# Kernel tuning notes

Measured on AMD Instinct MI355X. Metric: run time of the kernel, lower is better.

The kernel has to match this reference:

```python
import jax, jax.numpy as jnp
import numpy as np

N_NODES = 100000
N_EDGES = 800000
F_IN, HID, N_CLS = 256, 128, 32


def setup_inputs() -> dict:
    key = jax.random.key(0)
    k1, k2, k3, k4, k5 = jax.random.split(key, 5)
    features = jax.random.normal(k1, (N_NODES, F_IN), dtype=jnp.float32)
    # random directed edges with no self loops (so add_remaining_self_loops == append all loops)
    src = jax.random.randint(k2, (N_EDGES,), 0, N_NODES)
    off = jax.random.randint(k3, (N_EDGES,), 1, N_NODES)
    dst = (src + off) % N_NODES
    edge_index = jnp.stack([src, dst]).astype(jnp.int64)
    # Glorot-style params for the two GCNConv layers
    W1 = jax.random.normal(k4, (F_IN, HID), dtype=jnp.float32) * (1.0 / np.sqrt(F_IN))
    b1 = jnp.zeros((HID,), dtype=jnp.float32)
    W2 = jax.random.normal(k5, (HID, N_CLS), dtype=jnp.float32) * (1.0 / np.sqrt(HID))
    b2 = jnp.zeros((N_CLS,), dtype=jnp.float32)
    return {"features": features, "edge_index": edge_index, "W1": W1, "b1": b1, "W2": W2, "b2": b2}


def _gcn_conv(x, W, b, src, dst, norm, n):
    xw = x @ W                                  # [N, d_out] dense GEMM
    msg = xw[src] * norm[:, None]               # gather + scale, [E, d_out]
    out = jax.ops.segment_sum(msg, dst, num_segments=n)  # scatter-add to targets
    return out + b


def reference(features, edge_index, W1, b1, W2, b2):
    n = features.shape[0]
    # add_remaining_self_loops (input has none, so append all)
    loops = jnp.arange(n, dtype=edge_index.dtype)
    src = jnp.concatenate([edge_index[0], loops])
    dst = jnp.concatenate([edge_index[1], loops])
    # gcn_norm: deg over targets, sym normalization deg^-1/2 A deg^-1/2
    deg = jax.ops.segment_sum(jnp.ones_like(src, dtype=features.dtype), dst, num_segments=n)
    dinv = jnp.where(deg > 0, jax.lax.rsqrt(deg), 0.0)
    norm = dinv[src] * dinv[dst]
    x = _gcn_conv(features, W1, b1, src, dst, norm, n)
    x = jax.nn.relu(x)
    # dropout is identity at inference (training=False)
    x = _gcn_conv(x, W2, b2, src, dst, norm, n)
    return jax.nn.log_softmax(x, axis=1)
```

## Files before the change

### kernel.cpp

```cpp
#include <hip/hip_runtime.h>
#include <hip/hip_bf16.h>

typedef __bf16 bf16_t;
typedef __attribute__((ext_vector_type(8))) __bf16 bf16x8;
typedef __attribute__((ext_vector_type(4))) float f32x4;

__device__ inline void packB_one(const float* __restrict__ B, bf16_t* __restrict__ Bp,
                                 int N, int idx) {
    int j    = idx & 7;
    int lane = (idx >> 3) & 63;
    int st   = idx >> 9;
    int nt   = N >> 4;
    int s = st / nt, t = st - s * nt;
    int k = s * 32 + (lane >> 4) * 8 + j;
    int n = t * 16 + (lane & 15);
    Bp[idx] = (bf16_t)B[(size_t)k * N + n];
}

__global__ __launch_bounds__(256) void k_front(
        const float* __restrict__ feat, bf16_t* __restrict__ Ap,
        const float* __restrict__ W1, bf16_t* __restrict__ Bp1,
        const float* __restrict__ W2, bf16_t* __restrict__ Bp2,
        const int* __restrict__ dst, int* __restrict__ deg,
        int N_nodes, int E, int APACK_BLOCKS) {
    int b = blockIdx.x, t = threadIdx.x;
    if (b < APACK_BLOCKS) {
        int idx = b * 256 + t;
        if (idx >= N_nodes * 64) return;
        int w    = idx >> 6;
        int lane = idx & 63;
        int r16 = lane & 15, quad = lane >> 4;
        const float* arow = feat + (size_t)(w * 16 + r16) * 256 + quad * 8;
        bf16_t* opb = Ap + (size_t)w * 4096 + lane * 8;
#pragma unroll
        for (int s = 0; s < 8; ++s) {
            const float* ap = arow + s * 32;
            bf16x8 a;
#pragma unroll
            for (int j = 0; j < 8; ++j) a[j] = (bf16_t)ap[j];
            *(bf16x8*)(opb + s * 512) = a;
        }
        return;
    }
    b -= APACK_BLOCKS;
    const int PACK_BLOCKS = (32768 + 4096) / 256;
    if (b < PACK_BLOCKS) {
        int idx = b * 256 + t;
        if (idx < 32768) packB_one(W1, Bp1, 128, idx);
        else             packB_one(W2, Bp2, 32, idx - 32768);
        return;
    }
    int i = (b - PACK_BLOCKS) * 1024 + t * 4;
    if (i + 4 <= E) {
        int4 v = *(const int4*)(dst + i);
        atomicAdd(&deg[v.x], 1); atomicAdd(&deg[v.y], 1);
        atomicAdd(&deg[v.z], 1); atomicAdd(&deg[v.w], 1);
    } else {
#pragma unroll
        for (int j = 0; j < 4; ++j)
            if (i + j < E) atomicAdd(&deg[dst[i + j]], 1);
    }
}

__global__ __launch_bounds__(256) void k_dinv_scan1(const int* __restrict__ deg,
                                                    float* __restrict__ dinv,
                                                    int* __restrict__ bsum, int n) {
    __shared__ int red[256];
    int b = blockIdx.x, t = threadIdx.x;
    int base = b * 1024 + t * 4;
    int s = 0;
#pragma unroll
    for (int j = 0; j < 4; ++j) {
        int i = base + j;
        if (i < n) { int d = deg[i]; s += d; dinv[i] = rsqrtf((float)(d + 1)); }
    }
    red[t] = s;
    __syncthreads();
    for (int d = 128; d > 0; d >>= 1) {
        if (t < d) red[t] += red[t + d];
        __syncthreads();
    }
    if (t == 0) bsum[b] = red[0];
}

__global__ __launch_bounds__(256) void k_scan2(int* __restrict__ bsum, int nb,
                                               int* __restrict__ rowPtr, int n) {
    __shared__ int s[256];
    int t = threadIdx.x;
    int v = (t < nb) ? bsum[t] : 0;
    s[t] = v;
    __syncthreads();
    for (int d = 1; d < 256; d <<= 1) {
        int u = (t >= d) ? s[t - d] : 0;
        __syncthreads();
        s[t] += u;
        __syncthreads();
    }
    if (t < nb) bsum[t] = s[t] - v;
    if (t == 255) rowPtr[n] = s[255];
}

__global__ __launch_bounds__(256) void k_scan3(const int* __restrict__ deg,
                                               const int* __restrict__ bsum,
                                               int* __restrict__ rowPtr,
                                               int* __restrict__ cursor, int n) {
    __shared__ int red[256];
    int b = blockIdx.x, t = threadIdx.x;
    int base = b * 1024 + t * 4;
    int v[4]; int s = 0;
#pragma unroll
    for (int j = 0; j < 4; ++j) { int i = base + j; v[j] = (i < n) ? deg[i] : 0; s += v[j]; }
    red[t] = s;
    __syncthreads();
    for (int d = 1; d < 256; d <<= 1) {
        int u = (t >= d) ? red[t - d] : 0;
        __syncthreads();
        red[t] += u;
        __syncthreads();
    }
    int run = bsum[b] + red[t] - s;
#pragma unroll
    for (int j = 0; j < 4; ++j) {
        int i = base + j;
        if (i < n) { rowPtr[i] = run; cursor[i] = run; run += v[j]; }
    }
}

template <int KSTEPS, int NTILES>
__global__ __launch_bounds__(256) void k_gemm_scatter(
        const bf16_t* __restrict__ Ap, const bf16_t* __restrict__ Bp,
        bf16_t* __restrict__ C, int M, int gemmBlocks,
        const int* __restrict__ src, const int* __restrict__ dst,
        const float* __restrict__ dinv, int* __restrict__ cursor,
        int2* __restrict__ edata, int E) {
    int b = blockIdx.x, t = threadIdx.x;
    if (b < gemmBlocks) {
        int wave = (b * 256 + t) >> 6;
        if (wave * 16 >= M) return;
        int lane = t & 63;
        int r16 = lane & 15, quad = lane >> 4;
        const int N = NTILES * 16;
        f32x4 acc[NTILES] = {};
        const bf16_t* apb = Ap + (size_t)wave * (KSTEPS * 512) + lane * 8;
#pragma unroll
        for (int s = 0; s < KSTEPS; ++s) {
            bf16x8 a = *(const bf16x8*)(apb + s * 512);
            const bf16_t* bp = Bp + ((size_t)(s * NTILES) * 64 + lane) * 8;
#pragma unroll
            for (int tt = 0; tt < NTILES; ++tt) {
                bf16x8 bb = *(const bf16x8*)(bp + tt * 512);
                acc[tt] = __builtin_amdgcn_mfma_f32_16x16x32_bf16(a, bb, acc[tt], 0, 0, 0);
            }
        }
#pragma unroll
        for (int tt = 0; tt < NTILES; ++tt)
#pragma unroll
            for (int r = 0; r < 4; ++r)
                C[(size_t)(wave * 16 + quad * 4 + r) * N + tt * 16 + r16] = (bf16_t)acc[tt][r];
        return;
    }
    int e = (b - gemmBlocks) * 256 + t;
    if (e >= E) return;
    int s = src[e], d = dst[e];
    int pos = atomicAdd(&cursor[d], 1);
    int2 p; p.x = s; p.y = __float_as_int(dinv[s] * dinv[d]);
    edata[pos] = p;
}

template <int KSTEPS, int NTILES>
__global__ __launch_bounds__(256) void k_gemm_p(
        const bf16_t* __restrict__ Ap, const bf16_t* __restrict__ Bp,
        bf16_t* __restrict__ C, int M) {
    int wave = (blockIdx.x * blockDim.x + threadIdx.x) >> 6;
    if (wave * 16 >= M) return;
    int lane = threadIdx.x & 63;
    int r16 = lane & 15, quad = lane >> 4;
    const int N = NTILES * 16;
    f32x4 acc[NTILES] = {};
    const bf16_t* apb = Ap + (size_t)wave * (KSTEPS * 512) + lane * 8;
#pragma unroll
    for (int s = 0; s < KSTEPS; ++s) {
        bf16x8 a = *(const bf16x8*)(apb + s * 512);
        const bf16_t* bp = Bp + ((size_t)(s * NTILES) * 64 + lane) * 8;
#pragma unroll
        for (int t = 0; t < NTILES; ++t) {
            bf16x8 b = *(const bf16x8*)(bp + t * 512);
            acc[t] = __builtin_amdgcn_mfma_f32_16x16x32_bf16(a, b, acc[t], 0, 0, 0);
        }
    }
#pragma unroll
    for (int t = 0; t < NTILES; ++t)
#pragma unroll
        for (int r = 0; r < 4; ++r)
            C[(size_t)(wave * 16 + quad * 4 + r) * N + t * 16 + r16] = (bf16_t)acc[t][r];
}

__global__ __launch_bounds__(256) void k_agg1(
        const int* __restrict__ rowPtr, const int2* __restrict__ edata,
        const bf16_t* __restrict__ XW1, const float* __restrict__ dinv,
        const float* __restrict__ b1, bf16_t* __restrict__ Hp, int n) {
    int wave = (blockIdx.x * blockDim.x + threadIdx.x) >> 6;
    if (wave >= n) return;
    int lane = threadIdx.x & 63;
    int fl = (lane & 15) << 3;
    int h  = lane >> 4;
    int r0 = rowPtr[wave], r1 = rowPtr[wave + 1];
    float a0[8] = {}, a1[8] = {};
    int k = r0 + h;
    for (; k + 4 < r1; k += 8) {
        int2 e0 = edata[k], e1 = edata[k + 4];
        float w0 = __int_as_float(e0.y), w1 = __int_as_float(e1.y);
        bf16x8 x0 = *(const bf16x8*)(XW1 + ((size_t)e0.x << 7) + fl);
        bf16x8 x1 = *(const bf16x8*)(XW1 + ((size_t)e1.x << 7) + fl);
#pragma unroll
        for (int j = 0; j < 8; ++j) { a0[j] += (float)x0[j] * w0; a1[j] += (float)x1[j] * w1; }
    }
    if (k < r1) {
        int2 e0 = edata[k];
        float w0 = __int_as_float(e0.y);
        bf16x8 x0 = *(const bf16x8*)(XW1 + ((size_t)e0.x << 7) + fl);
#pragma unroll
        for (int j = 0; j < 8; ++j) a0[j] += (float)x0[j] * w0;
    }
#pragma unroll
    for (int j = 0; j < 8; ++j) {
        a0[j] += a1[j];
        a0[j] += __shfl_xor(a0[j], 16);
        a0[j] += __shfl_xor(a0[j], 32);
    }
    if (h == 0) {
        float d = dinv[wave], d2 = d * d;
        bf16x8 xs = *(const bf16x8*)(XW1 + ((size_t)wave << 7) + fl);
        bf16x8 hv;
#pragma unroll
        for (int j = 0; j < 8; ++j) {
            float v = a0[j] + (float)xs[j] * d2 + b1[fl + j];
            hv[j] = (bf16_t)fmaxf(v, 0.f);
        }
        int q = lane & 15;
        size_t off = (((size_t)(wave >> 4) * 4 + (q >> 2)) * 64
                      + (wave & 15) + 16 * (q & 3)) * 8;
        *(bf16x8*)(Hp + off) = hv;
    }
}

__global__ __launch_bounds__(256) void k_agg2(
        const int* __restrict__ rowPtr, const int2* __restrict__ edata,
        const bf16_t* __restrict__ XW2, const float* __restrict__ dinv,
        const float* __restrict__ b2, float* __restrict__ out, int n) {
    int wave = (blockIdx.x * blockDim.x + threadIdx.x) >> 6;
    if (wave >= n) return;
    int lane = threadIdx.x & 63;
    int g = lane & 15;
    int h = lane >> 4;
    int r0 = rowPtr[wave], r1 = rowPtr[wave + 1];
    float a00 = 0.f, a01 = 0.f, a10 = 0.f, a11 = 0.f;
    int k = r0 + h;
    for (; k + 4 < r1; k += 8) {
        int2 e0 = edata[k], e1 = edata[k + 4];
        float w0 = __int_as_float(e0.y), w1 = __int_as_float(e1.y);
        unsigned p0 = *(const unsigned*)(XW2 + ((size_t)e0.x << 5) + 2 * g);
        unsigned p1 = *(const unsigned*)(XW2 + ((size_t)e1.x << 5) + 2 * g);
        a00 += __int_as_float(p0 << 16) * w0;
        a01 += __int_as_float(p0 & 0xffff0000u) * w0;
        a10 += __int_as_float(p1 << 16) * w1;
        a11 += __int_as_float(p1 & 0xffff0000u) * w1;
    }
    if (k < r1) {
        int2 e0 = edata[k];
        float w0 = __int_as_float(e0.y);
        unsigned p0 = *(const unsigned*)(XW2 + ((size_t)e0.x << 5) + 2 * g);
        a00 += __int_as_float(p0 << 16) * w0;
        a01 += __int_as_float(p0 & 0xffff0000u) * w0;
    }
    float v0 = a00 + a10, v1 = a01 + a11;
    v0 += __shfl_xor(v0, 16); v0 += __shfl_xor(v0, 32);
    v1 += __shfl_xor(v1, 16); v1 += __shfl_xor(v1, 32);
    float d = dinv[wave], d2 = d * d;
    unsigned ps = *(const unsigned*)(XW2 + ((size_t)wave << 5) + 2 * g);
    float2 bb = *(const float2*)(b2 + 2 * g);
    v0 += __int_as_float(ps << 16) * d2 + bb.x;
    v1 += __int_as_float(ps & 0xffff0000u) * d2 + bb.y;
    float mx = fmaxf(v0, v1);
#pragma unroll
    for (int m = 8; m >= 1; m >>= 1) mx = fmaxf(mx, __shfl_xor(mx, m));
    float s = expf(v0 - mx) + expf(v1 - mx);
#pragma unroll
    for (int m = 8; m >= 1; m >>= 1) s += __shfl_xor(s, m);
    if (h == 0) {
        float ls = logf(s);
        float2 o; o.x = v0 - mx - ls; o.y = v1 - mx - ls;
        *(float2*)(out + ((size_t)wave << 5) + 2 * g) = o;
    }
}

extern "C" void kernel_launch(void* const* d_in, const int* in_sizes, int n_in,
                              void* d_out, int out_size, void* d_ws, size_t ws_size,
                              hipStream_t stream) {
    const float* feat = (const float*)d_in[0];
    const int*   eidx = (const int*)d_in[1];
    const float* W1   = (const float*)d_in[2];
    const float* b1   = (const float*)d_in[3];
    const float* W2   = (const float*)d_in[4];
    const float* b2   = (const float*)d_in[5];
    float* out = (float*)d_out;

    const int FIN = 256, HID = 128, NCLS = 32;
    const int N = in_sizes[0] / FIN;
    const int E = in_sizes[1] / 2;
    const int* src = eidx;
    const int* dst = eidx + E;

    char* ws = (char*)d_ws;
    size_t o = 0;
    auto alloc = [&](size_t bytes) -> void* {
        void* p = ws + o;
        o = (o + bytes + 255) & ~(size_t)255;
        return p;
    };
    int*    deg    = (int*)   alloc((size_t)N * 4);
    int*    cursor = (int*)   alloc((size_t)N * 4);
    float*  dinv   = (float*) alloc((size_t)N * 4);
    int*    rowPtr = (int*)   alloc((size_t)(N + 1) * 4);
    int*    bsum   = (int*)   alloc(256 * 4);
    bf16_t* Bp1    = (bf16_t*)alloc((size_t)(FIN / 32) * (HID / 16) * 512 * 2);
    bf16_t* Bp2    = (bf16_t*)alloc((size_t)(HID / 32) * (NCLS / 16) * 512 * 2);
    int2*   edata  = (int2*)  alloc((size_t)E * 8);
    bf16_t* Ap1    = (bf16_t*)alloc((size_t)N * FIN * 2);
    bf16_t* XW1    = (bf16_t*)alloc((size_t)N * HID * 2);
    bf16_t* Hp     = (bf16_t*)alloc((size_t)N * HID * 2);
    bf16_t* XW2    = XW1;

    const int T = 256;
    const int NB = (N + 1023) >> 10;
    const int APACK_BLOCKS = (N * 64 + T - 1) / T;
    const int AB = ((N / 16) * 64 + T - 1) / T;
    const int PACK_BLOCKS = (32768 + 4096) / 256;
    const int DEG_BLOCKS  = (E + 1023) / 1024;
    hipMemsetAsync(deg, 0, (size_t)N * 4, stream);
    k_front     <<<AB + PACK_BLOCKS + DEG_BLOCKS, T, 0, stream>>>(
        feat, Ap1, W1, Bp1, W2, Bp2, dst, deg, N / 16 * 16 * 4 , E, AB);
    k_dinv_scan1<<<NB, T, 0, stream>>>(deg, dinv, bsum, N);
    k_scan2     <<<1, T, 0, stream>>>(bsum, NB, rowPtr, N);
    k_scan3     <<<NB, T, 0, stream>>>(deg, bsum, rowPtr, cursor, N);

    {
        int waves = (N + 15) / 16;
        int gemmBlocks = (waves * 64 + T - 1) / T;
        int scatBlocks = (E + T - 1) / T;
        k_gemm_scatter<8, 8><<<gemmBlocks + scatBlocks, T, 0, stream>>>(
            Ap1, Bp1, XW1, N, gemmBlocks, src, dst, dinv, cursor, edata, E);
    }
    k_agg1<<<(N * 64 + T - 1) / T, T, 0, stream>>>(rowPtr, edata, XW1, dinv, b1, Hp, N);

    {
        int waves = (N + 15) / 16;
        k_gemm_p<4, 2><<<(waves * 64 + T - 1) / T, T, 0, stream>>>(Hp, Bp2, XW2, N);
    }
    k_agg2<<<(N * 64 + T - 1) / T, T, 0, stream>>>(rowPtr, edata, XW2, dinv, b2, out, N);
}
```

Baseline: 353.7 us.

## Record edge ranks during degree count to drop scatter atomics; fuse scan kernels

The degree-counting atomics now store their return value as each edge's rank within its destination. The CSR fill then computes positions as rowPtr[d]+rank with no second atomic pass, and processes four edges per thread with vector loads. The separate single-block scan kernel is folded into the third scan, where every block redundantly scans the block sums, which removes one launch and the cursor array. In exchange it writes and reads an extra E-sized rank array.

```diff
diff --git a/kernel.cpp b/kernel.cpp
--- a/kernel.cpp
+++ b/kernel.cpp
@@ -22,11 +22,11 @@
         const float* __restrict__ W1, bf16_t* __restrict__ Bp1,
         const float* __restrict__ W2, bf16_t* __restrict__ Bp2,
         const int* __restrict__ dst, int* __restrict__ deg,
-        int N_nodes, int E, int APACK_BLOCKS) {
+        int* __restrict__ rank, int apThreads, int E, int AB) {
     int b = blockIdx.x, t = threadIdx.x;
-    if (b < APACK_BLOCKS) {
+    if (b < AB) {
         int idx = b * 256 + t;
-        if (idx >= N_nodes * 64) return;
+        if (idx >= apThreads) return;
         int w    = idx >> 6;
         int lane = idx & 63;
         int r16 = lane & 15, quad = lane >> 4;
@@ -42,7 +42,7 @@
         }
         return;
     }
-    b -= APACK_BLOCKS;
+    b -= AB;
     const int PACK_BLOCKS = (32768 + 4096) / 256;
     if (b < PACK_BLOCKS) {
         int idx = b * 256 + t;
@@ -53,12 +53,15 @@
     int i = (b - PACK_BLOCKS) * 1024 + t * 4;
     if (i + 4 <= E) {
         int4 v = *(const int4*)(dst + i);
-        atomicAdd(&deg[v.x], 1); atomicAdd(&deg[v.y], 1);
-        atomicAdd(&deg[v.z], 1); atomicAdd(&deg[v.w], 1);
+        int4 r;
+        r.x = atomicAdd(&deg[v.x], 1);
+        r.y = atomicAdd(&deg[v.y], 1);
+        r.z = atomicAdd(&deg[v.z], 1);
+        r.w = atomicAdd(&deg[v.w], 1);
+        *(int4*)(rank + i) = r;
     } else {
-#pragma unroll
         for (int j = 0; j < 4; ++j)
-            if (i + j < E) atomicAdd(&deg[dst[i + j]], 1);
+            if (i + j < E) rank[i + j] = atomicAdd(&deg[dst[i + j]], 1);
     }
 }
 
@@ -83,46 +86,34 @@
     if (t == 0) bsum[b] = red[0];
 }
 
-__global__ __launch_bounds__(256) void k_scan2(int* __restrict__ bsum, int nb,
-                                               int* __restrict__ rowPtr, int n) {
-    __shared__ int s[256];
-    int t = threadIdx.x;
-    int v = (t < nb) ? bsum[t] : 0;
-    s[t] = v;
-    __syncthreads();
-    for (int d = 1; d < 256; d <<= 1) {
-        int u = (t >= d) ? s[t - d] : 0;
-        __syncthreads();
-        s[t] += u;
-        __syncthreads();
-    }
-    if (t < nb) bsum[t] = s[t] - v;
-    if (t == 255) rowPtr[n] = s[255];
-}
-
-__global__ __launch_bounds__(256) void k_scan3(const int* __restrict__ deg,
-                                               const int* __restrict__ bsum,
-                                               int* __restrict__ rowPtr,
-                                               int* __restrict__ cursor, int n) {
+__global__ __launch_bounds__(256) void k_scan3f(const int* __restrict__ deg,
+                                                const int* __restrict__ bsum, int nb,
+                                                int* __restrict__ rowPtr, int n) {
     __shared__ int red[256];
+    __shared__ int boff[256];
     int b = blockIdx.x, t = threadIdx.x;
     int base = b * 1024 + t * 4;
     int v[4]; int s = 0;
 #pragma unroll
     for (int j = 0; j < 4; ++j) { int i = base + j; v[j] = (i < n) ? deg[i] : 0; s += v[j]; }
     red[t] = s;
+    boff[t] = (t < nb) ? bsum[t] : 0;
     __syncthreads();
     for (int d = 1; d < 256; d <<= 1) {
-        int u = (t >= d) ? red[t - d] : 0;
+        int u  = (t >= d) ? red[t - d]  : 0;
+        int u2 = (t >= d) ? boff[t - d] : 0;
         __syncthreads();
         red[t] += u;
+        boff[t] += u2;
         __syncthreads();
     }
-    int run = bsum[b] + red[t] - s;
+    int blockOff = (b == 0) ? 0 : boff[b - 1];
+    if (b == 0 && t == 0) rowPtr[n] = boff[nb - 1];
+    int run = blockOff + red[t] - s;
 #pragma unroll
     for (int j = 0; j < 4; ++j) {
         int i = base + j;
-        if (i < n) { rowPtr[i] = run; cursor[i] = run; run += v[j]; }
+        if (i < n) { rowPtr[i] = run; run += v[j]; }
     }
 }
 
@@ -131,8 +122,8 @@
         const bf16_t* __restrict__ Ap, const bf16_t* __restrict__ Bp,
         bf16_t* __restrict__ C, int M, int gemmBlocks,
         const int* __restrict__ src, const int* __restrict__ dst,
-        const float* __restrict__ dinv, int* __restrict__ cursor,
-        int2* __restrict__ edata, int E) {
+        const int* __restrict__ rank, const int* __restrict__ rowPtr,
+        const float* __restrict__ dinv, int2* __restrict__ edata, int E) {
     int b = blockIdx.x, t = threadIdx.x;
     if (b < gemmBlocks) {
         int wave = (b * 256 + t) >> 6;
@@ -159,12 +150,27 @@
                 C[(size_t)(wave * 16 + quad * 4 + r) * N + tt * 16 + r16] = (bf16_t)acc[tt][r];
         return;
     }
-    int e = (b - gemmBlocks) * 256 + t;
-    if (e >= E) return;
-    int s = src[e], d = dst[e];
-    int pos = atomicAdd(&cursor[d], 1);
-    int2 p; p.x = s; p.y = __float_as_int(dinv[s] * dinv[d]);
-    edata[pos] = p;
+    int i = (b - gemmBlocks) * 1024 + t * 4;
+    if (i + 4 <= E) {
+        int4 s4 = *(const int4*)(src + i);
+        int4 d4 = *(const int4*)(dst + i);
+        int4 r4 = *(const int4*)(rank + i);
+        int p0 = rowPtr[d4.x] + r4.x, p1 = rowPtr[d4.y] + r4.y;
+        int p2 = rowPtr[d4.z] + r4.z, p3 = rowPtr[d4.w] + r4.w;
+        int2 e0; e0.x = s4.x; e0.y = __float_as_int(dinv[s4.x] * dinv[d4.x]);
+        int2 e1; e1.x = s4.y; e1.y = __float_as_int(dinv[s4.y] * dinv[d4.y]);
+        int2 e2; e2.x = s4.z; e2.y = __float_as_int(dinv[s4.z] * dinv[d4.z]);
+        int2 e3; e3.x = s4.w; e3.y = __float_as_int(dinv[s4.w] * dinv[d4.w]);
+        edata[p0] = e0; edata[p1] = e1; edata[p2] = e2; edata[p3] = e3;
+    } else {
+        for (int j = 0; j < 4; ++j) {
+            int e = i + j;
+            if (e >= E) break;
+            int s = src[e], d = dst[e];
+            int2 p; p.x = s; p.y = __float_as_int(dinv[s] * dinv[d]);
+            edata[rowPtr[d] + rank[e]] = p;
+        }
+    }
 }
 
 template <int KSTEPS, int NTILES>
@@ -319,7 +325,7 @@
         return p;
     };
     int*    deg    = (int*)   alloc((size_t)N * 4);
-    int*    cursor = (int*)   alloc((size_t)N * 4);
+    int*    rank   = (int*)   alloc((size_t)E * 4);
     float*  dinv   = (float*) alloc((size_t)N * 4);
     int*    rowPtr = (int*)   alloc((size_t)(N + 1) * 4);
     int*    bsum   = (int*)   alloc(256 * 4);
@@ -333,23 +339,22 @@
 
     const int T = 256;
     const int NB = (N + 1023) >> 10;
-    const int APACK_BLOCKS = (N * 64 + T - 1) / T;
-    const int AB = ((N / 16) * 64 + T - 1) / T;
+    const int apThreads = (N / 16) * 64;
+    const int AB = (apThreads + T - 1) / T;
     const int PACK_BLOCKS = (32768 + 4096) / 256;
     const int DEG_BLOCKS  = (E + 1023) / 1024;
     hipMemsetAsync(deg, 0, (size_t)N * 4, stream);
-    k_front     <<<AB + PACK_BLOCKS + DEG_BLOCKS, T, 0, stream>>>(
-        feat, Ap1, W1, Bp1, W2, Bp2, dst, deg, N / 16 * 16 * 4 , E, AB);
+    k_front<<<AB + PACK_BLOCKS + DEG_BLOCKS, T, 0, stream>>>(
+        feat, Ap1, W1, Bp1, W2, Bp2, dst, deg, rank, apThreads, E, AB);
     k_dinv_scan1<<<NB, T, 0, stream>>>(deg, dinv, bsum, N);
-    k_scan2     <<<1, T, 0, stream>>>(bsum, NB, rowPtr, N);
-    k_scan3     <<<NB, T, 0, stream>>>(deg, bsum, rowPtr, cursor, N);
+    k_scan3f    <<<NB, T, 0, stream>>>(deg, bsum, NB, rowPtr, N);
 
     {
         int waves = (N + 15) / 16;
         int gemmBlocks = (waves * 64 + T - 1) / T;
-        int scatBlocks = (E + T - 1) / T;
+        int scatBlocks = (E + 1023) / 1024;
         k_gemm_scatter<8, 8><<<gemmBlocks + scatBlocks, T, 0, stream>>>(
-            Ap1, Bp1, XW1, N, gemmBlocks, src, dst, dinv, cursor, edata, E);
+            Ap1, Bp1, XW1, N, gemmBlocks, src, dst, rank, rowPtr, dinv, edata, E);
     }
     k_agg1<<<(N * 64 + T - 1) / T, T, 0, stream>>>(rowPtr, edata, XW1, dinv, b1, Hp, N);
 
```

Measured after the change: 333.1 us. 5.8% less time.
